# Kernel optimization log

Hardware: AMD Instinct MI355X
Metric: run time of the kernel (lower is better)

## Reference

```python
import jax, jax.numpy as jnp
import numpy as np

HEADS = 16
DIM_HEAD = 64
EPS = 1e-5


def _layernorm(x, w, b):
    mu = jnp.mean(x, axis=-1, keepdims=True)
    var = jnp.var(x, axis=-1, keepdims=True)
    return (x - mu) * jax.lax.rsqrt(var + EPS) * w + b


def setup_inputs() -> dict:
    key = jax.random.key(0)
    ks = jax.random.split(key, 6)
    B, F, Q, D = 8, 4096, 64, 1024
    inner = HEADS * DIM_HEAD  # 1024
    s = 0.02
    return {
        "features": jax.random.normal(ks[0], (B, F, D), jnp.float32),
        "latents": jax.random.normal(ks[1], (B, Q, D), jnp.float32),
        "lnm_w": jnp.ones((D,), jnp.float32),
        "lnm_b": jnp.zeros((D,), jnp.float32),
        "lnl_w": jnp.ones((D,), jnp.float32),
        "lnl_b": jnp.zeros((D,), jnp.float32),
        "Wq": jax.random.normal(ks[2], (D, inner), jnp.float32) * s,
        "Wk": jax.random.normal(ks[3], (D, inner), jnp.float32) * s,
        "Wv": jax.random.normal(ks[4], (D, inner), jnp.float32) * s,
        "Wo": jax.random.normal(ks[5], (inner, D), jnp.float32) * s,
    }


def reference(features, latents, lnm_w, lnm_b, lnl_w, lnl_b, Wq, Wk, Wv, Wo):
    B, Q = latents.shape[0], latents.shape[1]
    scale = DIM_HEAD ** (-0.5)

    x = _layernorm(features, lnm_w, lnm_b)           # (B, F, D)
    lat = _layernorm(latents, lnl_w, lnl_b)          # (B, Q, D)

    q = (lat @ Wq).reshape(B, Q, HEADS, DIM_HEAD).transpose(0, 2, 1, 3)  # b h q d
    kv_in = jnp.concatenate([x, lat], axis=1)        # (B, F+Q, D)
    FL = kv_in.shape[1]
    k = (kv_in @ Wk).reshape(B, FL, HEADS, DIM_HEAD).transpose(0, 2, 1, 3)  # b h f d
    v = (kv_in @ Wv).reshape(B, FL, HEADS, DIM_HEAD).transpose(0, 2, 1, 3)  # b h f d

    sim = jnp.einsum('bhqd,bhfd->bhqf', q * scale, k)
    alphas = jax.nn.softmax(sim, axis=-1)            # amax-subtract is folded into stable softmax
    out = jnp.einsum('bhqf,bhfv->bhqv', alphas, v)
    out = out.transpose(0, 2, 1, 3).reshape(B, Q, HEADS * DIM_HEAD)
    return out @ Wo
```

## Files before the change

### kernel.cpp

```cpp
#include <hip/hip_runtime.h>


typedef float   f32x4  __attribute__((ext_vector_type(4)));
typedef short   bf16x8 __attribute__((ext_vector_type(8)));

#define MFMA_BF16 __builtin_amdgcn_mfma_f32_16x16x32_bf16

__device__ __forceinline__ unsigned short f2bf(float f) {
  unsigned u = __float_as_uint(f);
  unsigned r = (u + 0x7fffu + ((u >> 16) & 1u)) >> 16;
  return (unsigned short)r;
}

__device__ __forceinline__ void gload_lds16(const unsigned short* g, unsigned short* l) {
  __builtin_amdgcn_global_load_lds(
      (const __attribute__((address_space(1))) unsigned int*)g,
      (__attribute__((address_space(3))) unsigned int*)l, 16, 0, 0);
}

__global__ __launch_bounds__(256) void ln_kernel(
    const float* __restrict__ features, const float* __restrict__ latents,
    const float* __restrict__ lnm_w, const float* __restrict__ lnm_b,
    const float* __restrict__ lnl_w, const float* __restrict__ lnl_b,
    unsigned short* __restrict__ kv_ln, unsigned short* __restrict__ lat_ln)
{
  const int row = blockIdx.x;
  const int b  = row / 4160;
  const int fi = row - b * 4160;
  const bool is_lat = fi >= 4096;
  const float* x = is_lat ? (latents + (size_t)(b * 64 + fi - 4096) * 1024)
                          : (features + (size_t)(b * 4096 + fi) * 1024);
  const float* wp = is_lat ? lnl_w : lnm_w;
  const float* bp = is_lat ? lnl_b : lnm_b;
  const int tid = threadIdx.x;

  float4 v = *(const float4*)(x + tid * 4);
  float s  = v.x + v.y + v.z + v.w;
  float s2 = v.x * v.x + v.y * v.y + v.z * v.z + v.w * v.w;
#pragma unroll
  for (int sh = 1; sh < 64; sh <<= 1) {
    s  += __shfl_xor(s,  sh, 64);
    s2 += __shfl_xor(s2, sh, 64);
  }
  __shared__ float red[8];
  if ((tid & 63) == 0) { red[tid >> 6] = s; red[4 + (tid >> 6)] = s2; }
  __syncthreads();
  s  = red[0] + red[1] + red[2] + red[3];
  s2 = red[4] + red[5] + red[6] + red[7];
  const float mu   = s * (1.0f / 1024.0f);
  const float var  = s2 * (1.0f / 1024.0f) - mu * mu;
  const float rstd = rsqrtf(var + 1e-5f);

  float4 w4 = *(const float4*)(wp + tid * 4);
  float4 b4 = *(const float4*)(bp + tid * 4);
  ushort4 o;
  o.x = f2bf((v.x - mu) * rstd * w4.x + b4.x);
  o.y = f2bf((v.y - mu) * rstd * w4.y + b4.y);
  o.z = f2bf((v.z - mu) * rstd * w4.z + b4.z);
  o.w = f2bf((v.w - mu) * rstd * w4.w + b4.w);
  *(ushort4*)(kv_ln + (size_t)row * 1024 + tid * 4) = o;
  if (is_lat)
    *(ushort4*)(lat_ln + (size_t)(b * 64 + fi - 4096) * 1024 + tid * 4) = o;
}

__global__ __launch_bounds__(256) void wcast_kernel(
    const float* __restrict__ Wq, const float* __restrict__ Wk,
    const float* __restrict__ Wv, const float* __restrict__ Wo,
    unsigned short* __restrict__ Wkv_t, unsigned short* __restrict__ Wq_t,
    unsigned short* __restrict__ Wo_t)
{
  __shared__ float tile[32][33];
  const int kt = blockIdx.x * 32, nt = blockIdx.y * 32;
  const int tx = threadIdx.x & 31, ty = threadIdx.x >> 5;

  const float* src; int nc; float scale = 1.0f;
  if (nt < 1024)      { src = Wk; nc = nt; }
  else if (nt < 2048) { src = Wv; nc = nt - 1024; }
  else if (nt < 3072) { src = Wq; nc = nt - 2048; scale = 0.125f; }
  else                { src = Wo; nc = nt - 3072; }

#pragma unroll
  for (int kk = 0; kk < 4; ++kk)
    tile[ty + kk * 8][tx] = src[(size_t)(kt + ty + kk * 8) * 1024 + nc + tx] * scale;
  __syncthreads();

#pragma unroll
  for (int nn = 0; nn < 4; ++nn) {
    const int ng = nt + ty + nn * 8;
    unsigned short* d;
    if (ng < 2048)      d = Wkv_t + (size_t)ng * 1024;
    else if (ng < 3072) d = Wq_t + (size_t)(ng - 2048) * 1024;
    else                d = Wo_t + (size_t)(ng - 3072) * 1024;
    d[kt + tx] = f2bf(tile[tx][ty + nn * 8]);
  }
}

__global__ __launch_bounds__(512, 2) void gemm256_bf16(
    const unsigned short* __restrict__ A,
    const unsigned short* __restrict__ Bt,
    unsigned short* __restrict__ C, int M, int N, int K)
{
  __shared__ __align__(16) unsigned short lds[65536];
  const int tid  = threadIdx.x;
  const int wave = tid >> 6, lane = tid & 63;
  const int lo = lane & 15, hi = lane >> 4;
  const int wr = wave >> 2, wc = wave & 3;

  const int tilesN = N >> 8;
  const int perXcd = ((M >> 8) * tilesN) >> 3;
  const int xcd = blockIdx.x & 7, slot = blockIdx.x >> 3;
  const int ntw = (perXcd - slot + 31) >> 5;
  const int KT  = (K >> 6) * ntw;

  int g = xcd * perXcd + slot;
  int bm = g / tilesN;
  const int bn = g - bm * tilesN;

  int roff[2], coff[2];
#pragma unroll
  for (int gi = 0; gi < 2; ++gi) {
    int off = gi * 8192 + tid * 16;
    int p = off ^ (((off >> 9) & 1) << 5);
    int sub = (p >> 10) & 15;
    int q = p & 1023;
    roff[gi] = ((sub >> 1) << 4) + (q >> 6);
    coff[gi] = ((sub & 1) << 5) + ((q & 63) >> 1);
  }
  const unsigned short* pA[2];
  const unsigned short* pB[2];
#pragma unroll
  for (int gi = 0; gi < 2; ++gi) {
    pA[gi] = A  + (size_t)(bm * 256 + roff[gi]) * K + coff[gi];
    pB[gi] = Bt + (size_t)(bn * 256 + roff[gi]) * K + coff[gi];
  }
  const int halfStep  = 128 * K;
  const int tileStepA = 4 * 256 * K;

  f32x4 acc[8][4];
#pragma unroll
  for (int i = 0; i < 8; ++i)
#pragma unroll
    for (int j = 0; j < 4; ++j) acc[i][j] = (f32x4){0.f, 0.f, 0.f, 0.f};

#pragma unroll
  for (int ty = 0; ty < 4; ++ty) {
#pragma unroll
    for (int gi = 0; gi < 2; ++gi) {
      const unsigned short* src = (ty == 0) ? pA[gi]
                                : (ty == 1) ? pB[gi]
                                : (ty == 2) ? pA[gi] + halfStep
                                            : pB[gi] + halfStep;
      gload_lds16(src, lds + ty * 8192 + gi * 4096 + wave * 512);
    }
  }
  asm volatile("s_waitcnt vmcnt(6)" ::: "memory");
  asm volatile("s_barrier" ::: "memory");

  bf16x8 aLo[4][2], aHi[4][2], bLo[2][2], bHi[2][2];
  const int swz = (lo * 32 + hi * 8) ^ ((lo & 8) << 1);

  for (int kt = 0; kt < KT; ++kt) {
    const int t_local = kt & 15;
    const bool bnd = (t_local == 15);
    const bool st  = (kt + 1 < KT);
    const unsigned short* sb = lds + (kt & 1) * 32768;
    unsigned short*       db = lds + ((kt + 1) & 1) * 32768;
    const int offA = bnd ? tileStepA : ((t_local + 1) << 6);
    const int offB = bnd ? 0         : ((t_local + 1) << 6);

#pragma unroll
    for (int m = 0; m < 4; ++m)
#pragma unroll
      for (int ks = 0; ks < 2; ++ks)
        aLo[m][ks] = *(const bf16x8*)(sb + ((wr * 4 + m) * 2 + ks) * 512 + swz);
    if (st) {
#pragma unroll
      for (int gi = 0; gi < 2; ++gi)
        gload_lds16(pA[gi] + offA, db + gi * 4096 + wave * 512);
    }
    asm volatile("s_barrier" ::: "memory");
    asm volatile("s_waitcnt lgkmcnt(0)" ::: "memory");
    __builtin_amdgcn_sched_barrier(0);
    __builtin_amdgcn_s_setprio(1);
    if (t_local != 0) {
#pragma unroll
      for (int m = 0; m < 4; ++m)
#pragma unroll
        for (int n = 0; n < 2; ++n)
#pragma unroll
          for (int ks = 0; ks < 2; ++ks)
            acc[4 + m][2 + n] = MFMA_BF16(aHi[m][ks], bHi[n][ks], acc[4 + m][2 + n], 0, 0, 0);
    }
    __builtin_amdgcn_s_setprio(0);
    if (st) { asm volatile("s_waitcnt vmcnt(6)" ::: "memory"); }
    else    { asm volatile("s_waitcnt vmcnt(4)" ::: "memory"); }
    asm volatile("s_barrier" ::: "memory");

#pragma unroll
    for (int n = 0; n < 2; ++n)
#pragma unroll
      for (int ks = 0; ks < 2; ++ks)
        bLo[n][ks] = *(const bf16x8*)(sb + 8192 + ((wc * 2 + n) * 2 + ks) * 512 + swz);
    if (st) {
#pragma unroll
      for (int gi = 0; gi < 2; ++gi)
        gload_lds16(pB[gi] + offB, db + 8192 + gi * 4096 + wave * 512);
    }
    asm volatile("s_barrier" ::: "memory");
    asm volatile("s_waitcnt lgkmcnt(0)" ::: "memory");
    __builtin_amdgcn_sched_barrier(0);
    __builtin_amdgcn_s_setprio(1);
#pragma unroll
    for (int m = 0; m < 4; ++m)
#pragma unroll
      for (int n = 0; n < 2; ++n)
#pragma unroll
        for (int ks = 0; ks < 2; ++ks)
          acc[m][n] = MFMA_BF16(aLo[m][ks], bLo[n][ks], acc[m][n], 0, 0, 0);
    __builtin_amdgcn_s_setprio(0);
    if (st) { asm volatile("s_waitcnt vmcnt(6)" ::: "memory"); }
    else    { asm volatile("s_waitcnt vmcnt(2)" ::: "memory"); }
    asm volatile("s_barrier" ::: "memory");

#pragma unroll
    for (int m = 0; m < 4; ++m)
#pragma unroll
      for (int ks = 0; ks < 2; ++ks)
        aHi[m][ks] = *(const bf16x8*)(sb + 16384 + ((wr * 4 + m) * 2 + ks) * 512 + swz);
    if (st) {
#pragma unroll
      for (int gi = 0; gi < 2; ++gi)
        gload_lds16(pA[gi] + offA + halfStep, db + 16384 + gi * 4096 + wave * 512);
    }
    asm volatile("s_barrier" ::: "memory");
    asm volatile("s_waitcnt lgkmcnt(0)" ::: "memory");
    __builtin_amdgcn_sched_barrier(0);
    __builtin_amdgcn_s_setprio(1);
#pragma unroll
    for (int m = 0; m < 4; ++m)
#pragma unroll
      for (int n = 0; n < 2; ++n)
#pragma unroll
        for (int ks = 0; ks < 2; ++ks)
          acc[4 + m][n] = MFMA_BF16(aHi[m][ks], bLo[n][ks], acc[4 + m][n], 0, 0, 0);
    __builtin_amdgcn_s_setprio(0);
    if (st) { asm volatile("s_waitcnt vmcnt(6)" ::: "memory"); }
    else    { asm volatile("s_waitcnt vmcnt(0)" ::: "memory"); }
    asm volatile("s_barrier" ::: "memory");

#pragma unroll
    for (int n = 0; n < 2; ++n)
#pragma unroll
      for (int ks = 0; ks < 2; ++ks)
        bHi[n][ks] = *(const bf16x8*)(sb + 24576 + ((wc * 2 + n) * 2 + ks) * 512 + swz);
    if (st) {
#pragma unroll
      for (int gi = 0; gi < 2; ++gi)
        gload_lds16(pB[gi] + offB + halfStep, db + 24576 + gi * 4096 + wave * 512);
    }
    asm volatile("s_barrier" ::: "memory");
    asm volatile("s_waitcnt lgkmcnt(0)" ::: "memory");
    __builtin_amdgcn_sched_barrier(0);
    __builtin_amdgcn_s_setprio(1);
#pragma unroll
    for (int m = 0; m < 4; ++m)
#pragma unroll
      for (int n = 0; n < 2; ++n)
#pragma unroll
        for (int ks = 0; ks < 2; ++ks)
          acc[m][2 + n] = MFMA_BF16(aLo[m][ks], bHi[n][ks], acc[m][2 + n], 0, 0, 0);
    __builtin_amdgcn_s_setprio(0);
    if (st) { asm volatile("s_waitcnt vmcnt(6)" ::: "memory"); }
    asm volatile("s_barrier" ::: "memory");

    if (bnd) {
#pragma unroll
      for (int m = 0; m < 4; ++m)
#pragma unroll
        for (int n = 0; n < 2; ++n)
#pragma unroll
          for (int ks = 0; ks < 2; ++ks)
            acc[4 + m][2 + n] = MFMA_BF16(aHi[m][ks], bHi[n][ks], acc[4 + m][2 + n], 0, 0, 0);

#pragma unroll
      for (int i = 0; i < 8; ++i) {
        const int grow0 = bm * 256 + (i >> 2) * 128 + wr * 64 + (i & 3) * 16 + hi * 4;
#pragma unroll
        for (int j = 0; j < 4; ++j) {
          const int gcol = bn * 256 + (j >> 1) * 128 + wc * 32 + (j & 1) * 16 + lo;
#pragma unroll
          for (int r = 0; r < 4; ++r)
            C[(size_t)(grow0 + r) * N + gcol] = f2bf(acc[i][j][r]);
        }
      }
#pragma unroll
      for (int i = 0; i < 8; ++i)
#pragma unroll
        for (int j = 0; j < 4; ++j) acc[i][j] = (f32x4){0.f, 0.f, 0.f, 0.f};
      if (st) {
        pA[0] += tileStepA; pA[1] += tileStepA;
        bm += 4;
      }
    }
  }
}

template <typename CT>
__global__ __launch_bounds__(256) void gemm_tn(
    const unsigned short* __restrict__ A,
    const unsigned short* __restrict__ Bt,
    CT* __restrict__ C, int M, int N, int K)
{
  __shared__ __align__(16) unsigned short sA[2][128 * 32];
  __shared__ __align__(16) unsigned short sB[2][128 * 32];
  const int tid  = threadIdx.x;
  const int wave = tid >> 6, lane = tid & 63;
  const int bm = blockIdx.y, bn = blockIdx.x;
  const int wr = wave >> 1, wc = wave & 1;
  const int lo = lane & 15, hi = lane >> 4;
  const int srow = lane >> 2, squad = lane & 3;

  const unsigned short* gA = A  + (size_t)(bm * 128 + srow) * K + squad * 8;
  const unsigned short* gB = Bt + (size_t)(bn * 128 + srow) * K + squad * 8;

  f32x4 acc[4][4];
#pragma unroll
  for (int i = 0; i < 4; ++i)
#pragma unroll
    for (int j = 0; j < 4; ++j) acc[i][j] = (f32x4){0.f, 0.f, 0.f, 0.f};

  const int kt = K >> 5;
#pragma unroll
  for (int c = 0; c < 2; ++c) {
    const int chunk = wave * 2 + c;
    gload_lds16(gA + (size_t)chunk * 16 * K, &sA[0][chunk * 512]);
    gload_lds16(gB + (size_t)chunk * 16 * K, &sB[0][chunk * 512]);
  }
  __syncthreads();

  int buf = 0;
  for (int t = 0; t < kt; ++t) {
    if (t + 1 < kt) {
      const int k0 = (t + 1) << 5;
#pragma unroll
      for (int c = 0; c < 2; ++c) {
        const int chunk = wave * 2 + c;
        gload_lds16(gA + (size_t)chunk * 16 * K + k0, &sA[buf ^ 1][chunk * 512]);
        gload_lds16(gB + (size_t)chunk * 16 * K + k0, &sB[buf ^ 1][chunk * 512]);
      }
    }
    bf16x8 af[4], bfr[4];
#pragma unroll
    for (int i = 0; i < 4; ++i) {
      af[i]  = *(const bf16x8*)&sA[buf][(wr * 64 + i * 16 + lo) * 32 + hi * 8];
      bfr[i] = *(const bf16x8*)&sB[buf][(wc * 64 + i * 16 + lo) * 32 + hi * 8];
    }
#pragma unroll
    for (int i = 0; i < 4; ++i)
#pragma unroll
      for (int j = 0; j < 4; ++j)
        acc[i][j] = MFMA_BF16(af[i], bfr[j], acc[i][j], 0, 0, 0);
    __syncthreads();
    buf ^= 1;
  }

#pragma unroll
  for (int i = 0; i < 4; ++i) {
    const int row0 = bm * 128 + wr * 64 + i * 16 + hi * 4;
#pragma unroll
    for (int j = 0; j < 4; ++j) {
      const int col = bn * 128 + wc * 64 + j * 16 + lo;
#pragma unroll
      for (int r = 0; r < 4; ++r) {
        const size_t idx = (size_t)(row0 + r) * N + col;
        if constexpr (sizeof(CT) == 2) C[idx] = (CT)f2bf(acc[i][j][r]);
        else                            C[idx] = acc[i][j][r];
      }
    }
  }
}

__global__ __launch_bounds__(256) void attn_kernel(
    const unsigned short* __restrict__ qws,
    const unsigned short* __restrict__ KV,
    float* __restrict__ pacc, float* __restrict__ pml)
{
  const int bhs = blockIdx.x;
  const int s = bhs & 3, h = (bhs >> 2) & 15, b = bhs >> 6;
  const int t0 = (s * 65) >> 2;
  const int t1 = ((s + 1) * 65) >> 2;
  const int tid = threadIdx.x;
  const int wave = tid >> 6, lane = tid & 63;
  const int lo = lane & 15, hi = lane >> 4;

  __shared__ __align__(16) unsigned short sK [64][72];
  __shared__ __align__(16) unsigned short sVT[64][72];
  __shared__ __align__(16) unsigned short sP [4][16][72];

  bf16x8 qf[2];
  {
    const unsigned short* p = qws + (size_t)(b * 64 + wave * 16 + lo) * 1024 + h * 64 + hi * 8;
    qf[0] = *(const bf16x8*)p;
    qf[1] = *(const bf16x8*)(p + 32);
  }
  float m[4] = {-1e30f, -1e30f, -1e30f, -1e30f};
  float l[4] = {0.f, 0.f, 0.f, 0.f};
  f32x4 acc[4];
#pragma unroll
  for (int i = 0; i < 4; ++i) acc[i] = (f32x4){0.f, 0.f, 0.f, 0.f};

  const int frow = tid >> 2, c4 = tid & 3;

  bf16x8 kreg[2], vreg[2];
  {
    const size_t rb = (size_t)(b * 4160 + t0 * 64 + frow) * 2048 + h * 64;
#pragma unroll
    for (int rr = 0; rr < 2; ++rr) {
      const int d0 = rr * 32 + c4 * 8;
      kreg[rr] = *(const bf16x8*)(KV + rb + d0);
      vreg[rr] = *(const bf16x8*)(KV + rb + 1024 + d0);
    }
  }

  for (int t = t0; t < t1; ++t) {
    __syncthreads();
#pragma unroll
    for (int rr = 0; rr < 2; ++rr) {
      const int d0 = rr * 32 + c4 * 8;
      *(bf16x8*)&sK[frow][d0] = kreg[rr];
#pragma unroll
      for (int j = 0; j < 8; ++j) sVT[d0 + j][frow] = (unsigned short)vreg[rr][j];
    }
    __syncthreads();
    if (t + 1 < t1) {
      const size_t rb = (size_t)(b * 4160 + (t + 1) * 64 + frow) * 2048 + h * 64;
#pragma unroll
      for (int rr = 0; rr < 2; ++rr) {
        const int d0 = rr * 32 + c4 * 8;
        kreg[rr] = *(const bf16x8*)(KV + rb + d0);
        vreg[rr] = *(const bf16x8*)(KV + rb + 1024 + d0);
      }
    }

    f32x4 sim[4];
#pragma unroll
    for (int nf = 0; nf < 4; ++nf) {
      f32x4 a0 = (f32x4){0.f, 0.f, 0.f, 0.f};
#pragma unroll
      for (int ks = 0; ks < 2; ++ks) {
        bf16x8 kf = *(const bf16x8*)&sK[nf * 16 + lo][ks * 32 + hi * 8];
        a0 = MFMA_BF16(qf[ks], kf, a0, 0, 0, 0);
      }
      sim[nf] = a0;
    }

    float pr[4][4];
    float corr[4];
#pragma unroll
    for (int r = 0; r < 4; ++r) {
      float tm = fmaxf(fmaxf(sim[0][r], sim[1][r]), fmaxf(sim[2][r], sim[3][r]));
#pragma unroll
      for (int sh = 1; sh < 16; sh <<= 1) tm = fmaxf(tm, __shfl_xor(tm, sh, 64));
      const float mn = fmaxf(m[r], tm);
      corr[r] = __expf(m[r] - mn);
      float rs = 0.f;
#pragma unroll
      for (int nf = 0; nf < 4; ++nf) {
        float p = __expf(sim[nf][r] - mn);
        pr[r][nf] = p;
        rs += p;
      }
#pragma unroll
      for (int sh = 1; sh < 16; sh <<= 1) rs += __shfl_xor(rs, sh, 64);
      l[r] = l[r] * corr[r] + rs;
      m[r] = mn;
    }

    {
      const int r2 = lane & 3;
      float csel = r2 == 0 ? corr[0] : r2 == 1 ? corr[1] : r2 == 2 ? corr[2] : corr[3];
      const int src = ((lane & 15) >> 2) * 16 + (lane & 3);
      const float cacc = __shfl(csel, src, 64);
#pragma unroll
      for (int i = 0; i < 4; ++i) acc[i] *= cacc;
    }

#pragma unroll
    for (int r = 0; r < 4; ++r)
#pragma unroll
      for (int nf = 0; nf < 4; ++nf)
        sP[wave][hi * 4 + r][nf * 16 + lo] = f2bf(pr[r][nf]);

#pragma unroll
    for (int ks = 0; ks < 2; ++ks) {
      bf16x8 pf = *(const bf16x8*)&sP[wave][lo][ks * 32 + hi * 8];
#pragma unroll
      for (int i = 0; i < 4; ++i) {
        bf16x8 vf = *(const bf16x8*)&sVT[i * 16 + lo][ks * 32 + hi * 8];
        acc[i] = MFMA_BF16(vf, pf, acc[i], 0, 0, 0);
      }
    }
  }

  if (lo == 0) {
#pragma unroll
    for (int r = 0; r < 4; ++r) {
      pml[bhs * 128 + wave * 16 + hi * 4 + r]      = m[r];
      pml[bhs * 128 + 64 + wave * 16 + hi * 4 + r] = l[r];
    }
  }
#pragma unroll
  for (int i = 0; i < 4; ++i)
#pragma unroll
    for (int r = 0; r < 4; ++r)
      pacc[bhs * 4096 + (i * 16 + hi * 4 + r) * 64 + wave * 16 + lo] = acc[i][r];
}

__global__ __launch_bounds__(256) void attn_combine(
    const float* __restrict__ pacc, const float* __restrict__ pml,
    unsigned short* __restrict__ attn_out)
{
  const int bh = blockIdx.x;
  const int b = bh >> 4, h = bh & 15;
  const int t = threadIdx.x;
  const int q = t & 63, dg = t >> 6;
  const int base = bh << 2;

  float mm[4], ll[4];
#pragma unroll
  for (int s = 0; s < 4; ++s) {
    mm[s] = pml[(base + s) * 128 + q];
    ll[s] = pml[(base + s) * 128 + 64 + q];
  }
  float M = fmaxf(fmaxf(mm[0], mm[1]), fmaxf(mm[2], mm[3]));
  float e[4];
  float L = 0.f;
#pragma unroll
  for (int s = 0; s < 4; ++s) { e[s] = __expf(mm[s] - M); L += e[s] * ll[s]; }
  const float inv = 1.0f / L;

#pragma unroll
  for (int dd = 0; dd < 16; ++dd) {
    const int d = dg * 16 + dd;
    float v = 0.f;
#pragma unroll
    for (int s = 0; s < 4; ++s)
      v += e[s] * pacc[(base + s) * 4096 + d * 64 + q];
    attn_out[(size_t)(b * 64 + q) * 1024 + h * 64 + d] = f2bf(v * inv);
  }
}

extern "C" void kernel_launch(void* const* d_in, const int* in_sizes, int n_in,
                              void* d_out, int out_size, void* d_ws, size_t ws_size,
                              hipStream_t stream) {
  const float* features = (const float*)d_in[0];
  const float* latents  = (const float*)d_in[1];
  const float* lnm_w = (const float*)d_in[2];
  const float* lnm_b = (const float*)d_in[3];
  const float* lnl_w = (const float*)d_in[4];
  const float* lnl_b = (const float*)d_in[5];
  const float* Wq = (const float*)d_in[6];
  const float* Wk = (const float*)d_in[7];
  const float* Wv = (const float*)d_in[8];
  const float* Wo = (const float*)d_in[9];
  float* out = (float*)d_out;

  char* ws = (char*)d_ws;
  unsigned short* kv_ln    = (unsigned short*)(ws);
  unsigned short* Wkv_t    = (unsigned short*)(ws + 68157440);
  unsigned short* Wq_t     = (unsigned short*)(ws + 72351744);
  unsigned short* Wo_t     = (unsigned short*)(ws + 74448896);
  unsigned short* lat_ln   = (unsigned short*)(ws + 76546048);
  unsigned short* q_ws     = (unsigned short*)(ws + 77594624);
  unsigned short* attn_out = (unsigned short*)(ws + 78643200);
  unsigned short* KV       = (unsigned short*)(ws + 79691776);
  float* pacc = (float*)(ws);
  float* pml  = (float*)(ws + 8388608);

  ln_kernel<<<33280, 256, 0, stream>>>(features, latents, lnm_w, lnm_b, lnl_w, lnl_b,
                                       kv_ln, lat_ln);
  wcast_kernel<<<dim3(32, 128), 256, 0, stream>>>(Wq, Wk, Wv, Wo, Wkv_t, Wq_t, Wo_t);
  gemm256_bf16<<<256, 512, 0, stream>>>(kv_ln, Wkv_t, KV, 33280, 2048, 1024);
  gemm_tn<unsigned short><<<dim3(8, 4), 256, 0, stream>>>(lat_ln, Wq_t, q_ws, 512, 1024, 1024);
  attn_kernel<<<512, 256, 0, stream>>>(q_ws, KV, pacc, pml);
  attn_combine<<<128, 256, 0, stream>>>(pacc, pml, attn_out);
  gemm_tn<float><<<dim3(8, 4), 256, 0, stream>>>(attn_out, Wo_t, out, 512, 1024, 1024);
}
```

Before: 294.0 us.

## Write K/V as per-head planes and reorder GEMM phases with partial LDS waits

Measured after the change: 293.8 us. Within noise of the previous version (-0.1%).

```diff
diff --git a/kernel.cpp b/kernel.cpp
--- a/kernel.cpp
+++ b/kernel.cpp
@@ -98,7 +98,8 @@
 __global__ __launch_bounds__(512, 2) void gemm256_bf16(
     const unsigned short* __restrict__ A,
     const unsigned short* __restrict__ Bt,
-    unsigned short* __restrict__ C, int M, int N, int K)
+    unsigned short* __restrict__ Kp, unsigned short* __restrict__ Vp,
+    int M, int N, int K)
 {
   __shared__ __align__(16) unsigned short lds[65536];
   const int tid  = threadIdx.x;
@@ -148,8 +149,8 @@
     for (int gi = 0; gi < 2; ++gi) {
       const unsigned short* src = (ty == 0) ? pA[gi]
                                 : (ty == 1) ? pB[gi]
-                                : (ty == 2) ? pA[gi] + halfStep
-                                            : pB[gi] + halfStep;
+                                : (ty == 2) ? pB[gi] + halfStep
+                                            : pA[gi] + halfStep;
       gload_lds16(src, lds + ty * 8192 + gi * 4096 + wave * 512);
     }
   }
@@ -159,10 +160,12 @@
   bf16x8 aLo[4][2], aHi[4][2], bLo[2][2], bHi[2][2];
   const int swz = (lo * 32 + hi * 8) ^ ((lo & 8) << 1);
 
+#pragma unroll 2
   for (int kt = 0; kt < KT; ++kt) {
     const int t_local = kt & 15;
-    const bool bnd = (t_local == 15);
-    const bool st  = (kt + 1 < KT);
+    const bool first = (t_local == 0);
+    const bool bnd   = (t_local == 15);
+    const bool st    = (kt + 1 < KT);
     const unsigned short* sb = lds + (kt & 1) * 32768;
     unsigned short*       db = lds + ((kt + 1) & 1) * 32768;
     const int offA = bnd ? tileStepA : ((t_local + 1) << 6);
@@ -179,17 +182,17 @@
         gload_lds16(pA[gi] + offA, db + gi * 4096 + wave * 512);
     }
     asm volatile("s_barrier" ::: "memory");
-    asm volatile("s_waitcnt lgkmcnt(0)" ::: "memory");
+    asm volatile("s_waitcnt lgkmcnt(8)" ::: "memory");
     __builtin_amdgcn_sched_barrier(0);
     __builtin_amdgcn_s_setprio(1);
-    if (t_local != 0) {
+    if (!first) {
 #pragma unroll
       for (int m = 0; m < 4; ++m)
 #pragma unroll
         for (int n = 0; n < 2; ++n)
 #pragma unroll
           for (int ks = 0; ks < 2; ++ks)
-            acc[4 + m][2 + n] = MFMA_BF16(aHi[m][ks], bHi[n][ks], acc[4 + m][2 + n], 0, 0, 0);
+            acc[4 + m][n] = MFMA_BF16(aHi[m][ks], bLo[n][ks], acc[4 + m][n], 0, 0, 0);
     }
     __builtin_amdgcn_s_setprio(0);
     if (st) { asm volatile("s_waitcnt vmcnt(6)" ::: "memory"); }
@@ -207,7 +210,35 @@
         gload_lds16(pB[gi] + offB, db + 8192 + gi * 4096 + wave * 512);
     }
     asm volatile("s_barrier" ::: "memory");
-    asm volatile("s_waitcnt lgkmcnt(0)" ::: "memory");
+    asm volatile("s_waitcnt lgkmcnt(12)" ::: "memory");
+    __builtin_amdgcn_sched_barrier(0);
+    __builtin_amdgcn_s_setprio(1);
+    if (!first) {
+#pragma unroll
+      for (int m = 0; m < 4; ++m)
+#pragma unroll
+        for (int n = 0; n < 2; ++n)
+#pragma unroll
+          for (int ks = 0; ks < 2; ++ks)
+            acc[4 + m][2 + n] = MFMA_BF16(aHi[m][ks], bHi[n][ks], acc[4 + m][2 + n], 0, 0, 0);
+    }
+    __builtin_amdgcn_s_setprio(0);
+    if (st) { asm volatile("s_waitcnt vmcnt(6)" ::: "memory"); }
+    else    { asm volatile("s_waitcnt vmcnt(2)" ::: "memory"); }
+    asm volatile("s_barrier" ::: "memory");
+
+#pragma unroll
+    for (int n = 0; n < 2; ++n)
+#pragma unroll
+      for (int ks = 0; ks < 2; ++ks)
+        bHi[n][ks] = *(const bf16x8*)(sb + 16384 + ((wc * 2 + n) * 2 + ks) * 512 + swz);
+    if (st) {
+#pragma unroll
+      for (int gi = 0; gi < 2; ++gi)
+        gload_lds16(pB[gi] + offB + halfStep, db + 16384 + gi * 4096 + wave * 512);
+    }
+    asm volatile("s_barrier" ::: "memory");
+    asm volatile("s_waitcnt lgkmcnt(4)" ::: "memory");
     __builtin_amdgcn_sched_barrier(0);
     __builtin_amdgcn_s_setprio(1);
 #pragma unroll
@@ -219,47 +250,21 @@
           acc[m][n] = MFMA_BF16(aLo[m][ks], bLo[n][ks], acc[m][n], 0, 0, 0);
     __builtin_amdgcn_s_setprio(0);
     if (st) { asm volatile("s_waitcnt vmcnt(6)" ::: "memory"); }
-    else    { asm volatile("s_waitcnt vmcnt(2)" ::: "memory"); }
+    else    { asm volatile("s_waitcnt vmcnt(0)" ::: "memory"); }
     asm volatile("s_barrier" ::: "memory");
 
 #pragma unroll
     for (int m = 0; m < 4; ++m)
 #pragma unroll
       for (int ks = 0; ks < 2; ++ks)
-        aHi[m][ks] = *(const bf16x8*)(sb + 16384 + ((wr * 4 + m) * 2 + ks) * 512 + swz);
+        aHi[m][ks] = *(const bf16x8*)(sb + 24576 + ((wr * 4 + m) * 2 + ks) * 512 + swz);
     if (st) {
 #pragma unroll
       for (int gi = 0; gi < 2; ++gi)
-        gload_lds16(pA[gi] + offA + halfStep, db + 16384 + gi * 4096 + wave * 512);
-    }
-    asm volatile("s_barrier" ::: "memory");
-    asm volatile("s_waitcnt lgkmcnt(0)" ::: "memory");
-    __builtin_amdgcn_sched_barrier(0);
-    __builtin_amdgcn_s_setprio(1);
-#pragma unroll
-    for (int m = 0; m < 4; ++m)
-#pragma unroll
-      for (int n = 0; n < 2; ++n)
-#pragma unroll
-        for (int ks = 0; ks < 2; ++ks)
-          acc[4 + m][n] = MFMA_BF16(aHi[m][ks], bLo[n][ks], acc[4 + m][n], 0, 0, 0);
-    __builtin_amdgcn_s_setprio(0);
-    if (st) { asm volatile("s_waitcnt vmcnt(6)" ::: "memory"); }
-    else    { asm volatile("s_waitcnt vmcnt(0)" ::: "memory"); }
-    asm volatile("s_barrier" ::: "memory");
-
-#pragma unroll
-    for (int n = 0; n < 2; ++n)
-#pragma unroll
-      for (int ks = 0; ks < 2; ++ks)
-        bHi[n][ks] = *(const bf16x8*)(sb + 24576 + ((wc * 2 + n) * 2 + ks) * 512 + swz);
-    if (st) {
-#pragma unroll
-      for (int gi = 0; gi < 2; ++gi)
-        gload_lds16(pB[gi] + offB + halfStep, db + 24576 + gi * 4096 + wave * 512);
-    }
-    asm volatile("s_barrier" ::: "memory");
-    asm volatile("s_waitcnt lgkmcnt(0)" ::: "memory");
+        gload_lds16(pA[gi] + offA + halfStep, db + 24576 + gi * 4096 + wave * 512);
+    }
+    asm volatile("s_barrier" ::: "memory");
+    asm volatile("s_waitcnt lgkmcnt(8)" ::: "memory");
     __builtin_amdgcn_sched_barrier(0);
     __builtin_amdgcn_s_setprio(1);
 #pragma unroll
@@ -274,13 +279,17 @@
     asm volatile("s_barrier" ::: "memory");
 
     if (bnd) {
+      asm volatile("s_waitcnt lgkmcnt(0)" ::: "memory");
+      __builtin_amdgcn_sched_barrier(0);
 #pragma unroll
       for (int m = 0; m < 4; ++m)
 #pragma unroll
         for (int n = 0; n < 2; ++n)
 #pragma unroll
-          for (int ks = 0; ks < 2; ++ks)
+          for (int ks = 0; ks < 2; ++ks) {
+            acc[4 + m][n]     = MFMA_BF16(aHi[m][ks], bLo[n][ks], acc[4 + m][n], 0, 0, 0);
             acc[4 + m][2 + n] = MFMA_BF16(aHi[m][ks], bHi[n][ks], acc[4 + m][2 + n], 0, 0, 0);
+          }
 
 #pragma unroll
       for (int i = 0; i < 8; ++i) {
@@ -288,9 +297,11 @@
 #pragma unroll
         for (int j = 0; j < 4; ++j) {
           const int gcol = bn * 256 + (j >> 1) * 128 + wc * 32 + (j & 1) * 16 + lo;
+          unsigned short* plane = (gcol & 1024) ? Vp : Kp;
+          const size_t pbase = (size_t)((gcol >> 6) & 15) * 2129920 + (gcol & 63);
 #pragma unroll
           for (int r = 0; r < 4; ++r)
-            C[(size_t)(grow0 + r) * N + gcol] = f2bf(acc[i][j][r]);
+            plane[pbase + (size_t)(grow0 + r) * 64] = f2bf(acc[i][j][r]);
         }
       }
 #pragma unroll
@@ -382,7 +393,7 @@
 
 __global__ __launch_bounds__(256) void attn_kernel(
     const unsigned short* __restrict__ qws,
-    const unsigned short* __restrict__ KV,
+    const unsigned short* __restrict__ Kp, const unsigned short* __restrict__ Vp,
     float* __restrict__ pacc, float* __restrict__ pml)
 {
   const int bhs = blockIdx.x;
@@ -410,15 +421,16 @@
   for (int i = 0; i < 4; ++i) acc[i] = (f32x4){0.f, 0.f, 0.f, 0.f};
 
   const int frow = tid >> 2, c4 = tid & 3;
+  const size_t hbase = (size_t)h * 2129920;
 
   bf16x8 kreg[2], vreg[2];
   {
-    const size_t rb = (size_t)(b * 4160 + t0 * 64 + frow) * 2048 + h * 64;
+    const size_t rb = hbase + (size_t)(b * 4160 + t0 * 64 + frow) * 64;
 #pragma unroll
     for (int rr = 0; rr < 2; ++rr) {
       const int d0 = rr * 32 + c4 * 8;
-      kreg[rr] = *(const bf16x8*)(KV + rb + d0);
-      vreg[rr] = *(const bf16x8*)(KV + rb + 1024 + d0);
+      kreg[rr] = *(const bf16x8*)(Kp + rb + d0);
+      vreg[rr] = *(const bf16x8*)(Vp + rb + d0);
     }
   }
 
@@ -433,12 +445,12 @@
     }
     __syncthreads();
     if (t + 1 < t1) {
-      const size_t rb = (size_t)(b * 4160 + (t + 1) * 64 + frow) * 2048 + h * 64;
+      const size_t rb = hbase + (size_t)(b * 4160 + (t + 1) * 64 + frow) * 64;
 #pragma unroll
       for (int rr = 0; rr < 2; ++rr) {
         const int d0 = rr * 32 + c4 * 8;
-        kreg[rr] = *(const bf16x8*)(KV + rb + d0);
-        vreg[rr] = *(const bf16x8*)(KV + rb + 1024 + d0);
+        kreg[rr] = *(const bf16x8*)(Kp + rb + d0);
+        vreg[rr] = *(const bf16x8*)(Vp + rb + d0);
       }
     }
 
@@ -573,16 +585,17 @@
   unsigned short* lat_ln   = (unsigned short*)(ws + 76546048);
   unsigned short* q_ws     = (unsigned short*)(ws + 77594624);
   unsigned short* attn_out = (unsigned short*)(ws + 78643200);
-  unsigned short* KV       = (unsigned short*)(ws + 79691776);
+  unsigned short* Kp       = (unsigned short*)(ws + 79691776);
+  unsigned short* Vp       = (unsigned short*)(ws + 147849216);
   float* pacc = (float*)(ws);
   float* pml  = (float*)(ws + 8388608);
 
   ln_kernel<<<33280, 256, 0, stream>>>(features, latents, lnm_w, lnm_b, lnl_w, lnl_b,
                                        kv_ln, lat_ln);
   wcast_kernel<<<dim3(32, 128), 256, 0, stream>>>(Wq, Wk, Wv, Wo, Wkv_t, Wq_t, Wo_t);
-  gemm256_bf16<<<256, 512, 0, stream>>>(kv_ln, Wkv_t, KV, 33280, 2048, 1024);
+  gemm256_bf16<<<256, 512, 0, stream>>>(kv_ln, Wkv_t, Kp, Vp, 33280, 2048, 1024);
   gemm_tn<unsigned short><<<dim3(8, 4), 256, 0, stream>>>(lat_ln, Wq_t, q_ws, 512, 1024, 1024);
-  attn_kernel<<<512, 256, 0, stream>>>(q_ws, KV, pacc, pml);
+  attn_kernel<<<512, 256, 0, stream>>>(q_ws, Kp, Vp, pacc, pml);
   attn_combine<<<128, 256, 0, stream>>>(pacc, pml, attn_out);
   gemm_tn<float><<<dim3(8, 4), 256, 0, stream>>>(attn_out, Wo_t, out, 512, 1024, 1024);
 }
```
